# Kernel tuning notes

Hardware: AMD Instinct MI355X
Metric: run time of the kernel (lower is better)

## Reference

```python
import jax, jax.numpy as jnp
import numpy as np

T, H, I, E, K = 1024, 1024, 1024, 16, 4
ALPHA, LIMIT, EPS = 1.702, 7.0, 1e-5


def setup_inputs() -> dict:
    key = jax.random.key(0)
    ks = jax.random.split(key, 8)
    return {
        "x": jax.random.normal(ks[0], (T, H), jnp.float32),
        "norm_w": jnp.ones((H,), jnp.float32) + 0.01 * jax.random.normal(ks[1], (H,), jnp.float32),
        "router_w": 0.02 * jax.random.normal(ks[2], (E, H), jnp.float32),
        "router_b": jnp.zeros((E,), jnp.float32),
        "w13": 0.02 * jax.random.normal(ks[3], (E, H, 2 * I), jnp.float32),
        "b13": 0.01 * jax.random.normal(ks[4], (E, 2 * I), jnp.float32),
        "w2": 0.02 * jax.random.normal(ks[5], (E, I, H), jnp.float32),
        "b2": 0.01 * jax.random.normal(ks[6], (E, H), jnp.float32),
        "manual_weights": jnp.zeros((1, E), jnp.float32),  # zeros => override branch inactive, as in __init__
        "layer_idx": 0,
    }


def _override(g, lw):
    # torch: log_softmax, then force pos-masked experts to max+0.01, neg-masked to min-0.01
    gl = jax.nn.log_softmax(g, axis=-1)
    mx = jnp.max(gl, axis=-1, keepdims=True)
    mn = jnp.min(gl, axis=-1, keepdims=True)
    gl = jnp.where((lw > 0)[None, :], mx + 0.01, gl)
    gl = jnp.where((lw < 0)[None, :], mn - 0.01, gl)
    return gl


def reference(x, norm_w, router_w, router_b, w13, b13, w2, b2, manual_weights, layer_idx):
    # RMSNorm (eps=1e-5)
    t = x * jax.lax.rsqrt(jnp.mean(x * x, axis=-1, keepdims=True) + EPS) * norm_w
    # router logits [T, E]
    g = t @ router_w.T + router_b
    # conditional manual logit override
    lw = manual_weights[layer_idx]
    g = jax.lax.cond(jnp.max(jnp.abs(lw)) > 0,
                     lambda gg: _override(gg, lw),
                     lambda gg: gg, g)
    # top-k routing, renormalize=True (softmax -> topk -> renorm)
    probs = jax.nn.softmax(g, axis=-1)
    topw, topi = jax.lax.top_k(probs, K)
    topw = topw / jnp.sum(topw, axis=-1, keepdims=True)
    # dense combine matrix [T, E] (sparse dispatch in the fused kernel)
    combine = jnp.zeros(g.shape, x.dtype).at[jnp.arange(g.shape[0])[:, None], topi].add(topw)
    # expert compute: gate_up GEMM + swigluoai + down GEMM (dense over experts for the reference)
    h = jnp.einsum('th,ehf->tef', t, w13) + b13          # [T, E, 2I]
    gate = jnp.minimum(h[..., :I], LIMIT)                # clamp(max=limit)
    up = jnp.clip(h[..., I:], -LIMIT, LIMIT)             # clamp(-limit, limit)
    act = (up + 1.0) * gate * jax.nn.sigmoid(ALPHA * gate)
    y = jnp.einsum('tei,eih->teh', act, w2) + b2         # [T, E, H]
    moe = jnp.einsum('te,teh->th', combine, y)           # weighted scatter-combine
    return x + moe
```

## Files before the change

kernel.cpp:

```cpp
#include <hip/hip_runtime.h>

#define T_    1024
#define H_    1024
#define IDIM  1024
#define E_    16
#define TOPK  4
#define ALPHA 1.702f
#define LIMIT 7.0f

typedef __bf16 bf16;
typedef __bf16 bf16x4 __attribute__((ext_vector_type(4)));
typedef __bf16 bf16x8 __attribute__((ext_vector_type(8)));
typedef float  f32x4  __attribute__((ext_vector_type(4)));

__global__ __launch_bounds__(256) void k_rms_router(
    const float* __restrict__ x, const float* __restrict__ nw,
    const float* __restrict__ rw, const float* __restrict__ rb,
    const float* __restrict__ mw, const int* __restrict__ lidx,
    bf16* __restrict__ tB, float* __restrict__ out,
    int* __restrict__ cnt, int* __restrict__ tok_list,
    float* __restrict__ wgt_list)
{
    const int t = blockIdx.x, tid = threadIdx.x;
    const int lane = tid & 63, wave = tid >> 6;
    __shared__ float tbuf[H_];
    __shared__ float red[4];
    __shared__ float logits[E_];

    float4 xv = ((const float4*)(x + (size_t)t * H_))[tid];
    float4 wv = ((const float4*)nw)[tid];
    float ssq = xv.x*xv.x + xv.y*xv.y + xv.z*xv.z + xv.w*xv.w;
    #pragma unroll
    for (int off = 32; off; off >>= 1) ssq += __shfl_xor(ssq, off);
    if (lane == 0) red[wave] = ssq;
    __syncthreads();
    const float rms = rsqrtf((red[0] + red[1] + red[2] + red[3]) * (1.0f / H_) + 1e-5f);

    float4 tv;
    tv.x = xv.x * rms * wv.x;
    tv.y = xv.y * rms * wv.y;
    tv.z = xv.z * rms * wv.z;
    tv.w = xv.w * rms * wv.w;

    ((float4*)(out + (size_t)t * H_))[tid] = xv;
    ((float4*)tbuf)[tid] = tv;
    bf16x4 tb = { (bf16)tv.x, (bf16)tv.y, (bf16)tv.z, (bf16)tv.w };
    *(bf16x4*)(tB + (size_t)t * H_ + tid * 4) = tb;
    __syncthreads();

    #pragma unroll
    for (int ei = 0; ei < 4; ++ei) {
        const int e = wave * 4 + ei;
        const float* wr = rw + (size_t)e * H_;
        float s = 0.f;
        #pragma unroll
        for (int j = 0; j < 16; ++j) {
            const int c = lane + j * 64;
            s += tbuf[c] * wr[c];
        }
        #pragma unroll
        for (int off = 32; off; off >>= 1) s += __shfl_xor(s, off);
        if (lane == 0) logits[e] = s + rb[e];
    }
    __syncthreads();

    if (tid == 0) {
        float g[E_];
        #pragma unroll
        for (int e = 0; e < E_; ++e) g[e] = logits[e];

        const int li = lidx[0];
        float ma = 0.f, lw[E_];
        #pragma unroll
        for (int e = 0; e < E_; ++e) { lw[e] = mw[li * E_ + e]; ma = fmaxf(ma, fabsf(lw[e])); }
        if (ma > 0.f) {
            float mx = -1e30f;
            for (int e = 0; e < E_; ++e) mx = fmaxf(mx, g[e]);
            float se = 0.f;
            for (int e = 0; e < E_; ++e) se += expf(g[e] - mx);
            const float lse = logf(se) + mx;
            float gl[E_], gmx = -1e30f, gmn = 1e30f;
            for (int e = 0; e < E_; ++e) { gl[e] = g[e] - lse; gmx = fmaxf(gmx, gl[e]); gmn = fminf(gmn, gl[e]); }
            for (int e = 0; e < E_; ++e) {
                if (lw[e] > 0.f)      gl[e] = gmx + 0.01f;
                else if (lw[e] < 0.f) gl[e] = gmn - 0.01f;
                g[e] = gl[e];
            }
        }

        float mx = -1e30f;
        #pragma unroll
        for (int e = 0; e < E_; ++e) mx = fmaxf(mx, g[e]);
        float p[E_];
        #pragma unroll
        for (int e = 0; e < E_; ++e) p[e] = expf(g[e] - mx);

        bool used[E_] = {};
        int   idx[TOPK];
        float twv[TOPK];
        float ssum = 0.f;
        for (int k = 0; k < TOPK; ++k) {
            int best = -1; float bv = -1e30f;
            for (int e = 0; e < E_; ++e)
                if (!used[e] && p[e] > bv) { bv = p[e]; best = e; }
            used[best] = true; idx[k] = best; twv[k] = bv; ssum += bv;
        }
        const float inv = 1.f / ssum;
        for (int k = 0; k < TOPK; ++k) {
            const int e = idx[k];
            const int slot = atomicAdd(&cnt[e], 1);
            tok_list[e * T_ + slot] = t;
            wgt_list[e * T_ + slot] = twv[k] * inv;
        }
    }
}

__global__ void k_scan(const int* __restrict__ cnt, int* __restrict__ base)
{
    if (threadIdx.x == 0) {
        int s = 0;
        for (int e = 0; e < E_; ++e) { base[e] = s; s += cnt[e]; }
        base[E_] = s;
    }
}

__global__ __launch_bounds__(256) void k_gateup(
    const bf16* __restrict__ tB, const float* __restrict__ w13,
    const float* __restrict__ b13, const int* __restrict__ cnt,
    const int* __restrict__ base, const int* __restrict__ tok_list,
    bf16* __restrict__ act)
{
    const int e  = blockIdx.z;
    const int ne = cnt[e];
    const int m0 = blockIdx.y * 64;
    if (m0 >= ne) return;
    const int n0  = blockIdx.x * 64;
    const int tid = threadIdx.x, lane = tid & 63, wave = tid >> 6;

    __shared__ __align__(16) bf16 As[64][40];
    __shared__ __align__(16) bf16 Bg[64][40];
    __shared__ __align__(16) bf16 Bu[64][40];
    __shared__ int stok[64];

    if (tid < 64) {
        const int s = m0 + tid;
        stok[tid] = (s < ne) ? tok_list[e * T_ + s] : -1;
    }
    __syncthreads();

    const int ar = tid >> 2, ak = (tid & 3) * 8;
    const int atok = stok[ar];
    const int bn = tid & 63, bk = wave * 8;
    const size_t wrow = (size_t)(2 * IDIM);
    const float* wbase = w13 + (size_t)e * H_ * wrow + n0 + bn;

    const int wm = wave >> 1, wn = wave & 1;
    const int q = lane >> 4, r = lane & 15;
    f32x4 accg[2][2] = {};
    f32x4 accu[2][2] = {};

    for (int kb = 0; kb < H_ / 32; ++kb) {
        __syncthreads();
        uint4 av = make_uint4(0u, 0u, 0u, 0u);
        if (atok >= 0)
            av = *(const uint4*)(tB + (size_t)atok * H_ + kb * 32 + ak);
        *(uint4*)&As[ar][ak] = av;
        {
            const float* src = wbase + (size_t)(kb * 32 + bk) * wrow;
            bf16x8 pg, pu;
            #pragma unroll
            for (int j = 0; j < 8; ++j) {
                pg[j] = (bf16)src[(size_t)j * wrow];
                pu[j] = (bf16)src[(size_t)j * wrow + IDIM];
            }
            *(bf16x8*)&Bg[bn][bk] = pg;
            *(bf16x8*)&Bu[bn][bk] = pu;
        }
        __syncthreads();
        bf16x8 a[2], bg[2], bu[2];
        a[0]  = *(const bf16x8*)&As[wm * 32 +      r][q * 8];
        a[1]  = *(const bf16x8*)&As[wm * 32 + 16 + r][q * 8];
        bg[0] = *(const bf16x8*)&Bg[wn * 32 +      r][q * 8];
        bg[1] = *(const bf16x8*)&Bg[wn * 32 + 16 + r][q * 8];
        bu[0] = *(const bf16x8*)&Bu[wn * 32 +      r][q * 8];
        bu[1] = *(const bf16x8*)&Bu[wn * 32 + 16 + r][q * 8];
        #pragma unroll
        for (int im = 0; im < 2; ++im)
            #pragma unroll
            for (int in = 0; in < 2; ++in) {
                accg[im][in] = __builtin_amdgcn_mfma_f32_16x16x32_bf16(a[im], bg[in], accg[im][in], 0, 0, 0);
                accu[im][in] = __builtin_amdgcn_mfma_f32_16x16x32_bf16(a[im], bu[in], accu[im][in], 0, 0, 0);
            }
    }

    const int sb = base[e];
    #pragma unroll
    for (int im = 0; im < 2; ++im) {
        #pragma unroll
        for (int in = 0; in < 2; ++in) {
            #pragma unroll
            for (int rg = 0; rg < 4; ++rg) {
                const int row = wm * 32 + im * 16 + q * 4 + rg;
                const int col = wn * 32 + in * 16 + r;
                if (m0 + row < ne) {
                    const float hg = accg[im][in][rg] + b13[e * 2 * IDIM + n0 + col];
                    const float hu = accu[im][in][rg] + b13[e * 2 * IDIM + IDIM + n0 + col];
                    const float gt = fminf(hg, LIMIT);
                    const float up = fminf(fmaxf(hu, -LIMIT), LIMIT);
                    const float av = (up + 1.0f) * gt / (1.0f + expf(-ALPHA * gt));
                    act[(size_t)(sb + m0 + row) * IDIM + n0 + col] = (bf16)av;
                }
            }
        }
    }
}

__global__ __launch_bounds__(256) void k_down(
    const bf16* __restrict__ act, const float* __restrict__ w2,
    const float* __restrict__ b2, const int* __restrict__ cnt,
    const int* __restrict__ base, const int* __restrict__ tok_list,
    const float* __restrict__ wgt_list, float* __restrict__ out)
{
    const int e  = blockIdx.z;
    const int ne = cnt[e];
    const int m0 = blockIdx.y * 64;
    if (m0 >= ne) return;
    const int n0  = blockIdx.x * 64;
    const int tid = threadIdx.x, lane = tid & 63, wave = tid >> 6;

    __shared__ __align__(16) bf16 As[64][40];
    __shared__ __align__(16) bf16 Bs[64][40];
    __shared__ int   stok[64];
    __shared__ float swgt[64];

    if (tid < 64) {
        const int s = m0 + tid;
        stok[tid] = (s < ne) ? tok_list[e * T_ + s] : -1;
        swgt[tid] = (s < ne) ? wgt_list[e * T_ + s] : 0.f;
    }
    __syncthreads();

    const int sb = base[e];
    const int ar = tid >> 2, ak = (tid & 3) * 8;
    const bool arow_ok = (m0 + ar) < ne;
    const int bn = tid & 63, bk = wave * 8;
    const float* wbase = w2 + (size_t)e * IDIM * H_ + n0 + bn;

    const int wm = wave >> 1, wn = wave & 1;
    const int q = lane >> 4, r = lane & 15;
    f32x4 acc[2][2] = {};

    for (int kb = 0; kb < IDIM / 32; ++kb) {
        __syncthreads();
        uint4 av = make_uint4(0u, 0u, 0u, 0u);
        if (arow_ok)
            av = *(const uint4*)(act + (size_t)(sb + m0 + ar) * IDIM + kb * 32 + ak);
        *(uint4*)&As[ar][ak] = av;
        {
            const float* src = wbase + (size_t)(kb * 32 + bk) * H_;
            bf16x8 pb;
            #pragma unroll
            for (int j = 0; j < 8; ++j) pb[j] = (bf16)src[(size_t)j * H_];
            *(bf16x8*)&Bs[bn][bk] = pb;
        }
        __syncthreads();
        bf16x8 a[2], b[2];
        a[0] = *(const bf16x8*)&As[wm * 32 +      r][q * 8];
        a[1] = *(const bf16x8*)&As[wm * 32 + 16 + r][q * 8];
        b[0] = *(const bf16x8*)&Bs[wn * 32 +      r][q * 8];
        b[1] = *(const bf16x8*)&Bs[wn * 32 + 16 + r][q * 8];
        #pragma unroll
        for (int im = 0; im < 2; ++im)
            #pragma unroll
            for (int in = 0; in < 2; ++in)
                acc[im][in] = __builtin_amdgcn_mfma_f32_16x16x32_bf16(a[im], b[in], acc[im][in], 0, 0, 0);
    }

    #pragma unroll
    for (int im = 0; im < 2; ++im) {
        #pragma unroll
        for (int in = 0; in < 2; ++in) {
            #pragma unroll
            for (int rg = 0; rg < 4; ++rg) {
                const int row = wm * 32 + im * 16 + q * 4 + rg;
                const int col = wn * 32 + in * 16 + r;
                if (m0 + row < ne) {
                    const int   tok = stok[row];
                    const float w   = swgt[row];
                    const float v   = w * (acc[im][in][rg] + b2[e * H_ + n0 + col]);
                    atomicAdd(&out[(size_t)tok * H_ + n0 + col], v);
                }
            }
        }
    }
}

extern "C" void kernel_launch(void* const* d_in, const int* in_sizes, int n_in,
                              void* d_out, int out_size, void* d_ws, size_t ws_size,
                              hipStream_t stream)
{
    const float* x        = (const float*)d_in[0];
    const float* norm_w   = (const float*)d_in[1];
    const float* router_w = (const float*)d_in[2];
    const float* router_b = (const float*)d_in[3];
    const float* w13      = (const float*)d_in[4];
    const float* b13      = (const float*)d_in[5];
    const float* w2       = (const float*)d_in[6];
    const float* b2       = (const float*)d_in[7];
    const float* manual_w = (const float*)d_in[8];
    const int*   layer_i  = (const int*)d_in[9];
    float* out = (float*)d_out;

    char* ws = (char*)d_ws;
    bf16*  tB       = (bf16*)ws;
    bf16*  act      = (bf16*)(ws + (2u << 20));
    int*   cnt      = (int*)(ws + (10u << 20));
    int*   basep    = cnt + E_;
    int*   tok_list = (int*)(ws + (10u << 20) + 256);
    float* wgt_list = (float*)(ws + (10u << 20) + 256 + (64u << 10));

    hipMemsetAsync(cnt, 0, E_ * sizeof(int), stream);

    k_rms_router<<<T_, 256, 0, stream>>>(x, norm_w, router_w, router_b,
                                         manual_w, layer_i, tB, out,
                                         cnt, tok_list, wgt_list);
    k_scan<<<1, 64, 0, stream>>>(cnt, basep);

    dim3 gg(IDIM / 64, T_ / 64, E_);
    k_gateup<<<gg, 256, 0, stream>>>(tB, w13, b13, cnt, basep, tok_list, act);

    dim3 gd(H_ / 64, T_ / 64, E_);
    k_down<<<gd, 256, 0, stream>>>(act, w2, b2, cnt, basep, tok_list, wgt_list, out);
}
```

Measured before the change: 408.0 us.

## Repack expert weights into MFMA-fragment bf16 layout and stream GEMMs without LDS

Adds a repack kernel that converts fp32 w13 and w2 into bf16 tiles laid out in MFMA B-fragment order. New gate-up and down kernels then load A and B fragments straight from global memory into registers with double buffering, skipping LDS and barriers, and give each wave larger 64x32 tiles. The goal is to remove the strided fp32 weight loads, the per-tile conversion and the shared-memory staging of the old kernels. In exchange every call repacks all weights, which adds traffic, and the path only runs when the workspace is at least 108 MB; otherwise the old kernels are used.

```diff
diff --git a/kernel.cpp b/kernel.cpp
--- a/kernel.cpp
+++ b/kernel.cpp
@@ -124,6 +124,200 @@
     }
 }
 
+__global__ __launch_bounds__(256) void k_repack(
+    const float* __restrict__ W, bf16* __restrict__ out, int Ndim)
+{
+    __shared__ float tile[32][260];
+    const int e = blockIdx.z, kb = blockIdx.y, n0 = blockIdx.x * 256;
+    const int t = threadIdx.x;
+    const int nbs = Ndim >> 4;
+
+    const float* src = W + ((size_t)e * 1024 + (size_t)kb * 32) * Ndim + n0;
+    #pragma unroll
+    for (int i = 0; i < 8; ++i) {
+        const int idx = i * 256 + t;
+        const int k = idx >> 6, c4 = (idx & 63) * 4;
+        float4 v = *(const float4*)(src + (size_t)k * Ndim + c4);
+        *(float4*)&tile[k][c4] = v;
+    }
+    __syncthreads();
+
+    const int f = t >> 4;
+    const int lg = (t & 15) * 4;
+    bf16* dst = out + (((size_t)(e * nbs + n0 / 16 + f)) * 32 + kb) * 512;
+    #pragma unroll
+    for (int li = 0; li < 4; ++li) {
+        const int l = lg + li, q = l >> 4, r = l & 15;
+        bf16x8 p;
+        #pragma unroll
+        for (int j = 0; j < 8; ++j) p[j] = (bf16)tile[q * 8 + j][f * 16 + r];
+        *(bf16x8*)(dst + l * 8) = p;
+    }
+}
+
+__global__ __launch_bounds__(256) void k_gateup2(
+    const bf16* __restrict__ tB, const bf16* __restrict__ w13p,
+    const float* __restrict__ b13, const int* __restrict__ cnt,
+    const int* __restrict__ base, const int* __restrict__ tok_list,
+    bf16* __restrict__ act)
+{
+    const int e  = blockIdx.z;
+    const int ne = cnt[e];
+    const int m0 = blockIdx.y * 64;
+    if (m0 >= ne) return;
+    const int wave = threadIdx.x >> 6, lane = threadIdx.x & 63;
+    const int q = lane >> 4, r = lane & 15;
+    const int nb0 = blockIdx.x * 8 + wave * 2;
+
+    const bf16* pA0; const bf16* pA1; const bf16* pA2; const bf16* pA3;
+    {
+        const int* tl = tok_list + e * T_;
+        int s0 = m0 + 0  + r; s0 = s0 < ne ? s0 : ne - 1;
+        int s1 = m0 + 16 + r; s1 = s1 < ne ? s1 : ne - 1;
+        int s2 = m0 + 32 + r; s2 = s2 < ne ? s2 : ne - 1;
+        int s3 = m0 + 48 + r; s3 = s3 < ne ? s3 : ne - 1;
+        pA0 = tB + (size_t)tl[s0] * H_ + q * 8;
+        pA1 = tB + (size_t)tl[s1] * H_ + q * 8;
+        pA2 = tB + (size_t)tl[s2] * H_ + q * 8;
+        pA3 = tB + (size_t)tl[s3] * H_ + q * 8;
+    }
+    const bf16* pBg0 = w13p + ((size_t)(e * 128 + nb0     ) * 32) * 512 + lane * 8;
+    const bf16* pBg1 = w13p + ((size_t)(e * 128 + nb0 + 1 ) * 32) * 512 + lane * 8;
+    const bf16* pBu0 = w13p + ((size_t)(e * 128 + nb0 + 64) * 32) * 512 + lane * 8;
+    const bf16* pBu1 = w13p + ((size_t)(e * 128 + nb0 + 65) * 32) * 512 + lane * 8;
+
+    f32x4 accg[4][2] = {};
+    f32x4 accu[4][2] = {};
+    bf16x8 a0[4], b0[4], a1[4], b1[4];
+
+#define LOADG(A, B) do { \
+    A[0] = *(const bf16x8*)pA0; pA0 += 32; \
+    A[1] = *(const bf16x8*)pA1; pA1 += 32; \
+    A[2] = *(const bf16x8*)pA2; pA2 += 32; \
+    A[3] = *(const bf16x8*)pA3; pA3 += 32; \
+    B[0] = *(const bf16x8*)pBg0; pBg0 += 512; \
+    B[1] = *(const bf16x8*)pBg1; pBg1 += 512; \
+    B[2] = *(const bf16x8*)pBu0; pBu0 += 512; \
+    B[3] = *(const bf16x8*)pBu1; pBu1 += 512; } while (0)
+
+#define COMPG(A, B) do { \
+    _Pragma("unroll") \
+    for (int mf = 0; mf < 4; ++mf) { \
+        accg[mf][0] = __builtin_amdgcn_mfma_f32_16x16x32_bf16(A[mf], B[0], accg[mf][0], 0, 0, 0); \
+        accg[mf][1] = __builtin_amdgcn_mfma_f32_16x16x32_bf16(A[mf], B[1], accg[mf][1], 0, 0, 0); \
+        accu[mf][0] = __builtin_amdgcn_mfma_f32_16x16x32_bf16(A[mf], B[2], accu[mf][0], 0, 0, 0); \
+        accu[mf][1] = __builtin_amdgcn_mfma_f32_16x16x32_bf16(A[mf], B[3], accu[mf][1], 0, 0, 0); \
+    } } while (0)
+
+    LOADG(a0, b0);
+    for (int kb = 0; kb < 30; kb += 2) {
+        LOADG(a1, b1); COMPG(a0, b0);
+        LOADG(a0, b0); COMPG(a1, b1);
+    }
+    LOADG(a1, b1); COMPG(a0, b0); COMPG(a1, b1);
+#undef LOADG
+#undef COMPG
+
+    const int sb = base[e];
+    #pragma unroll
+    for (int mf = 0; mf < 4; ++mf) {
+        #pragma unroll
+        for (int nf = 0; nf < 2; ++nf) {
+            const int cg = (nb0 + nf) * 16 + r;
+            const float bg = b13[e * 2 * IDIM + cg];
+            const float bu = b13[e * 2 * IDIM + IDIM + cg];
+            #pragma unroll
+            for (int rg = 0; rg < 4; ++rg) {
+                const int row = mf * 16 + q * 4 + rg;
+                if (m0 + row < ne) {
+                    const float hg = accg[mf][nf][rg] + bg;
+                    const float hu = accu[mf][nf][rg] + bu;
+                    const float gt = fminf(hg, LIMIT);
+                    const float up = fminf(fmaxf(hu, -LIMIT), LIMIT);
+                    const float av = (up + 1.0f) * gt / (1.0f + expf(-ALPHA * gt));
+                    act[(size_t)(sb + m0 + row) * IDIM + cg] = (bf16)av;
+                }
+            }
+        }
+    }
+}
+
+__global__ __launch_bounds__(256) void k_down2(
+    const bf16* __restrict__ act, const bf16* __restrict__ w2p,
+    const float* __restrict__ b2, const int* __restrict__ cnt,
+    const int* __restrict__ base, const int* __restrict__ tok_list,
+    const float* __restrict__ wgt_list, float* __restrict__ out)
+{
+    const int e  = blockIdx.z;
+    const int ne = cnt[e];
+    const int m0 = blockIdx.y * 64;
+    if (m0 >= ne) return;
+    const int sb = base[e];
+    const int wave = threadIdx.x >> 6, lane = threadIdx.x & 63;
+    const int q = lane >> 4, r = lane & 15;
+    const int nb0 = blockIdx.x * 8 + wave * 2;
+
+    const bf16* pA0; const bf16* pA1; const bf16* pA2; const bf16* pA3;
+    {
+        int s0 = m0 + 0  + r; s0 = s0 < ne ? s0 : ne - 1;
+        int s1 = m0 + 16 + r; s1 = s1 < ne ? s1 : ne - 1;
+        int s2 = m0 + 32 + r; s2 = s2 < ne ? s2 : ne - 1;
+        int s3 = m0 + 48 + r; s3 = s3 < ne ? s3 : ne - 1;
+        pA0 = act + (size_t)(sb + s0) * IDIM + q * 8;
+        pA1 = act + (size_t)(sb + s1) * IDIM + q * 8;
+        pA2 = act + (size_t)(sb + s2) * IDIM + q * 8;
+        pA3 = act + (size_t)(sb + s3) * IDIM + q * 8;
+    }
+    const bf16* pB0 = w2p + ((size_t)(e * 64 + nb0    ) * 32) * 512 + lane * 8;
+    const bf16* pB1 = w2p + ((size_t)(e * 64 + nb0 + 1) * 32) * 512 + lane * 8;
+
+    f32x4 acc[4][2] = {};
+    bf16x8 a0[4], b0[2], a1[4], b1[2];
+
+#define LOADD(A, B) do { \
+    A[0] = *(const bf16x8*)pA0; pA0 += 32; \
+    A[1] = *(const bf16x8*)pA1; pA1 += 32; \
+    A[2] = *(const bf16x8*)pA2; pA2 += 32; \
+    A[3] = *(const bf16x8*)pA3; pA3 += 32; \
+    B[0] = *(const bf16x8*)pB0; pB0 += 512; \
+    B[1] = *(const bf16x8*)pB1; pB1 += 512; } while (0)
+
+#define COMPD(A, B) do { \
+    _Pragma("unroll") \
+    for (int mf = 0; mf < 4; ++mf) { \
+        acc[mf][0] = __builtin_amdgcn_mfma_f32_16x16x32_bf16(A[mf], B[0], acc[mf][0], 0, 0, 0); \
+        acc[mf][1] = __builtin_amdgcn_mfma_f32_16x16x32_bf16(A[mf], B[1], acc[mf][1], 0, 0, 0); \
+    } } while (0)
+
+    LOADD(a0, b0);
+    for (int kb = 0; kb < 30; kb += 2) {
+        LOADD(a1, b1); COMPD(a0, b0);
+        LOADD(a0, b0); COMPD(a1, b1);
+    }
+    LOADD(a1, b1); COMPD(a0, b0); COMPD(a1, b1);
+#undef LOADD
+#undef COMPD
+
+    #pragma unroll
+    for (int mf = 0; mf < 4; ++mf) {
+        #pragma unroll
+        for (int nf = 0; nf < 2; ++nf) {
+            const int ch = (nb0 + nf) * 16 + r;
+            const float bb = b2[e * H_ + ch];
+            #pragma unroll
+            for (int rg = 0; rg < 4; ++rg) {
+                const int row = mf * 16 + q * 4 + rg;
+                const int s = m0 + row;
+                if (s < ne) {
+                    const int   tok = tok_list[e * T_ + s];
+                    const float w   = wgt_list[e * T_ + s];
+                    atomicAdd(&out[(size_t)tok * H_ + ch], w * (acc[mf][nf][rg] + bb));
+                }
+            }
+        }
+    }
+}
+
 __global__ __launch_bounds__(256) void k_gateup(
     const bf16* __restrict__ tB, const float* __restrict__ w13,
     const float* __restrict__ b13, const int* __restrict__ cnt,
@@ -195,9 +389,9 @@
 
     const int sb = base[e];
     #pragma unroll
-    for (int im = 0; im < 2; ++im) {
-        #pragma unroll
-        for (int in = 0; in < 2; ++in) {
+    for (int im = 0; im < 2; ++im)
+        #pragma unroll
+        for (int in = 0; in < 2; ++in)
             #pragma unroll
             for (int rg = 0; rg < 4; ++rg) {
                 const int row = wm * 32 + im * 16 + q * 4 + rg;
@@ -211,8 +405,6 @@
                     act[(size_t)(sb + m0 + row) * IDIM + n0 + col] = (bf16)av;
                 }
             }
-        }
-    }
 }
 
 __global__ __launch_bounds__(256) void k_down(
@@ -277,9 +469,9 @@
     }
 
     #pragma unroll
-    for (int im = 0; im < 2; ++im) {
-        #pragma unroll
-        for (int in = 0; in < 2; ++in) {
+    for (int im = 0; im < 2; ++im)
+        #pragma unroll
+        for (int in = 0; in < 2; ++in)
             #pragma unroll
             for (int rg = 0; rg < 4; ++rg) {
                 const int row = wm * 32 + im * 16 + q * 4 + rg;
@@ -287,12 +479,9 @@
                 if (m0 + row < ne) {
                     const int   tok = stok[row];
                     const float w   = swgt[row];
-                    const float v   = w * (acc[im][in][rg] + b2[e * H_ + n0 + col]);
-                    atomicAdd(&out[(size_t)tok * H_ + n0 + col], v);
+                    atomicAdd(&out[(size_t)tok * H_ + n0 + col], w * (acc[im][in][rg] + b2[e * H_ + n0 + col]));
                 }
             }
-        }
-    }
 }
 
 extern "C" void kernel_launch(void* const* d_in, const int* in_sizes, int n_in,
@@ -313,11 +502,15 @@
 
     char* ws = (char*)d_ws;
     bf16*  tB       = (bf16*)ws;
-    bf16*  act      = (bf16*)(ws + (2u << 20));
-    int*   cnt      = (int*)(ws + (10u << 20));
+    bf16*  act      = (bf16*)(ws + (2ull << 20));
+    int*   cnt      = (int*)(ws + (10ull << 20));
     int*   basep    = cnt + E_;
-    int*   tok_list = (int*)(ws + (10u << 20) + 256);
-    float* wgt_list = (float*)(ws + (10u << 20) + 256 + (64u << 10));
+    int*   tok_list = (int*)(ws + (10ull << 20) + 256);
+    float* wgt_list = (float*)(ws + (10ull << 20) + 256 + (64ull << 10));
+    bf16*  w13p     = (bf16*)(ws + (12ull << 20));
+    bf16*  w2p      = (bf16*)(ws + (76ull << 20));
+
+    const bool fast = ws_size >= (108ull << 20);
 
     hipMemsetAsync(cnt, 0, E_ * sizeof(int), stream);
 
@@ -326,9 +519,20 @@
                                          cnt, tok_list, wgt_list);
     k_scan<<<1, 64, 0, stream>>>(cnt, basep);
 
-    dim3 gg(IDIM / 64, T_ / 64, E_);
-    k_gateup<<<gg, 256, 0, stream>>>(tB, w13, b13, cnt, basep, tok_list, act);
-
-    dim3 gd(H_ / 64, T_ / 64, E_);
-    k_down<<<gd, 256, 0, stream>>>(act, w2, b2, cnt, basep, tok_list, wgt_list, out);
-}
+    if (fast) {
+        dim3 gr13(2 * IDIM / 256, 32, E_);
+        k_repack<<<gr13, 256, 0, stream>>>(w13, w13p, 2 * IDIM);
+        dim3 gr2(H_ / 256, 32, E_);
+        k_repack<<<gr2, 256, 0, stream>>>(w2, w2p, H_);
+
+        dim3 gg(8, 16, E_);
+        k_gateup2<<<gg, 256, 0, stream>>>(tB, w13p, b13, cnt, basep, tok_list, act);
+        dim3 gd(8, 16, E_);
+        k_down2<<<gd, 256, 0, stream>>>(act, w2p, b2, cnt, basep, tok_list, wgt_list, out);
+    } else {
+        dim3 gg(IDIM / 64, T_ / 64, E_);
+        k_gateup<<<gg, 256, 0, stream>>>(tB, w13, b13, cnt, basep, tok_list, act);
+        dim3 gd(H_ / 64, T_ / 64, E_);
+        k_down<<<gd, 256, 0, stream>>>(act, w2, b2, cnt, basep, tok_list, wgt_list, out);
+    }
+}
```

New measurement: 484.8 us. 18.8% more time.
